# Kernel optimization log

Measured on AMD Instinct MI355X. Metric: run time of the kernel, lower is better.

The kernel has to match this reference:

```python
import jax, jax.numpy as jnp
import numpy as np

N = 50000
E = 800000
F_IN = 128
HID = 64
HEADS = 4
NEG_SLOPE = 0.2  # PyG GATConv default negative_slope


def segment_softmax(e, dst, num_segments):
    # numerically stable softmax over edges grouped by destination node
    m = jax.ops.segment_max(e, dst, num_segments=num_segments)
    ex = jnp.exp(e - m[dst])
    s = jax.ops.segment_sum(ex, dst, num_segments=num_segments)
    return ex / (s[dst] + 1e-16)


def gat_conv(x, src, dst, W, a_src, a_dst, bias, heads, out_ch, concat):
    n = x.shape[0]
    h = (x @ W).reshape(n, heads, out_ch)          # [N,H,C]
    alpha_s = (h * a_src).sum(-1)                  # [N,H]
    alpha_d = (h * a_dst).sum(-1)                  # [N,H]
    e = jax.nn.leaky_relu(alpha_s[src] + alpha_d[dst], NEG_SLOPE)  # [E,H]
    alpha = segment_softmax(e, dst, n)             # [E,H]
    out = jax.ops.segment_sum(h[src] * alpha[:, :, None], dst, num_segments=n)  # [N,H,C]
    out = out.reshape(n, heads * out_ch) if concat else out.mean(axis=1)
    return out + bias


def setup_inputs() -> dict:
    key = jax.random.key(0)
    ks = jax.random.split(key, 16)

    def lin(k, i, o):
        return (jax.random.normal(k, (i, o), jnp.float32) / np.float32(np.sqrt(i)))

    def att(k, h, c):
        return jax.random.normal(k, (h, c), jnp.float32) * np.float32(0.1)

    x = jax.random.normal(ks[0], (N, F_IN), jnp.float32)
    edge_index = jax.random.randint(ks[1], (2, E), 0, N, dtype=jnp.int32)
    return {
        "x": x,
        "W_emb": lin(ks[2], F_IN, HID), "b_emb": jnp.zeros(HID, jnp.float32),
        "W0": lin(ks[3], HID, HEADS * HID), "as0": att(ks[4], HEADS, HID), "ad0": att(ks[5], HEADS, HID), "b0": jnp.zeros(HEADS * HID, jnp.float32),
        "W1": lin(ks[6], HEADS * HID, HEADS * HID), "as1": att(ks[7], HEADS, HID), "ad1": att(ks[8], HEADS, HID), "b1": jnp.zeros(HEADS * HID, jnp.float32),
        "W2": lin(ks[9], HEADS * HID, HID), "as2": att(ks[10], 1, HID), "ad2": att(ks[11], 1, HID), "b2": jnp.zeros(HID, jnp.float32),
        "Wo1": lin(ks[12], HID, HID // 2), "bo1": jnp.zeros(HID // 2, jnp.float32),
        "Wo2": lin(ks[13], HID // 2, 1), "bo2": jnp.zeros(1, jnp.float32),
        "edge_index": edge_index,
    }


def reference(x, W_emb, b_emb, W0, as0, ad0, b0, W1, as1, ad1, b1, W2, as2, ad2, b2, Wo1, bo1, Wo2, bo2, edge_index):
    n = x.shape[0]
    loop = jnp.arange(n, dtype=edge_index.dtype)  # PyG GATConv adds self-loops
    src = jnp.concatenate([edge_index[0], loop])
    dst = jnp.concatenate([edge_index[1], loop])
    h = jax.nn.relu(x @ W_emb + b_emb)
    h = jax.nn.relu(gat_conv(h, src, dst, W0, as0, ad0, b0, HEADS, HID, True))   # dropout=identity (eval)
    h = jax.nn.relu(gat_conv(h, src, dst, W1, as1, ad1, b1, HEADS, HID, True))
    h = gat_conv(h, src, dst, W2, as2, ad2, b2, 1, HID, False)
    h = jax.nn.relu(h @ Wo1 + bo1)
    return h @ Wo2 + bo2  # [N,1]
```

## Files before the change

### kernel.cpp

```cpp
#include <hip/hip_runtime.h>

typedef _Float16 h8_t __attribute__((ext_vector_type(8)));
typedef _Float16 h4_t __attribute__((ext_vector_type(4)));
typedef float floatx4 __attribute__((ext_vector_type(4)));

__device__ __forceinline__ float leaky(float v) { return v >= 0.f ? v : 0.2f * v; }

__global__ void hist_kernel(const int* __restrict__ dst, int E, int* __restrict__ cnt) {
    int e = blockIdx.x * blockDim.x + threadIdx.x;
    if (e < E) atomicAdd(&cnt[dst[e]], 1);
}

__global__ __launch_bounds__(256) void blocksum_kernel(const int* __restrict__ cnt, int N,
                                                       int* __restrict__ bsum) {
    __shared__ int red[256];
    int tid = threadIdx.x;
    int idx = blockIdx.x * 256 + tid;
    red[tid] = idx < N ? cnt[idx] + 1 : 0;
    __syncthreads();
#pragma unroll
    for (int off = 128; off >= 1; off >>= 1) {
        if (tid < off) red[tid] += red[tid + off];
        __syncthreads();
    }
    if (tid == 0) bsum[blockIdx.x] = red[0];
}

__global__ __launch_bounds__(256) void scanbsum_kernel(int* __restrict__ bsum, int nb,
                                                       int* __restrict__ total) {
    __shared__ int part[256];
    int tid = threadIdx.x;
    int per = (nb + 255) / 256;
    int s0 = tid * per, s1 = min(s0 + per, nb);
    int s = 0;
    for (int i = s0; i < s1; i++) s += bsum[i];
    part[tid] = s;
    __syncthreads();
    for (int off = 1; off < 256; off <<= 1) {
        int v = (tid >= off) ? part[tid - off] : 0;
        __syncthreads();
        part[tid] += v;
        __syncthreads();
    }
    int base = (tid == 0) ? 0 : part[tid - 1];
    for (int i = s0; i < s1; i++) {
        int v = bsum[i];
        bsum[i] = base;
        base += v;
    }
    if (tid == 255) *total = part[255];
}

__global__ __launch_bounds__(256) void rowptr_kernel(const int* __restrict__ cnt,
                                                     const int* __restrict__ bsum, int N,
                                                     int* __restrict__ row_ptr,
                                                     int* __restrict__ cursor) {
    __shared__ int lds[256];
    int tid = threadIdx.x;
    int idx = blockIdx.x * 256 + tid;
    int v = idx < N ? cnt[idx] + 1 : 0;
    lds[tid] = v;
    __syncthreads();
    for (int off = 1; off < 256; off <<= 1) {
        int t = (tid >= off) ? lds[tid - off] : 0;
        __syncthreads();
        lds[tid] += t;
        __syncthreads();
    }
    if (idx < N) {
        int p = bsum[blockIdx.x] + lds[tid] - v;
        row_ptr[idx] = p;
        cursor[idx] = p;
    }
}

__global__ void scatter_kernel(const int* __restrict__ src, const int* __restrict__ dst,
                               int E, int N, int* __restrict__ cursor, int* __restrict__ csr_src) {
    int e = blockIdx.x * blockDim.x + threadIdx.x;
    if (e >= E + N) return;
    int s, d;
    if (e < E) { s = src[e]; d = dst[e]; }
    else       { s = e - E;  d = s; }
    int pos = atomicAdd(&cursor[d], 1);
    csr_src[pos] = s;
}

__global__ void prep_weights_all(const float* __restrict__ W_emb, const float* __restrict__ W0,
                                 const float* __restrict__ W1, const float* __restrict__ W2,
                                 _Float16* __restrict__ WeH, _Float16* __restrict__ WeL,
                                 _Float16* __restrict__ W0H, _Float16* __restrict__ W0L,
                                 _Float16* __restrict__ W1H, _Float16* __restrict__ W1L,
                                 _Float16* __restrict__ W2H, _Float16* __restrict__ W2L) {
    int which = blockIdx.y;
    const float* W;
    _Float16 *Wh, *Wl;
    int K, N;
    if (which == 0)      { W = W_emb; Wh = WeH; Wl = WeL; K = 128; N = 64; }
    else if (which == 1) { W = W0;    Wh = W0H; Wl = W0L; K = 64;  N = 256; }
    else if (which == 2) { W = W1;    Wh = W1H; Wl = W1L; K = 256; N = 256; }
    else                 { W = W2;    Wh = W2H; Wl = W2L; K = 256; N = 64; }
    int idx = blockIdx.x * blockDim.x + threadIdx.x;
    if (idx >= K * N) return;
    int k = idx / N, n = idx % N;
    float v = W[idx];
    _Float16 hi = (_Float16)v;
    _Float16 lo = (_Float16)(v - (float)hi);
    size_t o = ((size_t)(k >> 3) * N + n) * 8 + (k & 7);
    Wh[o] = hi; Wl[o] = lo;
}

__global__ __launch_bounds__(256) void gemm_emb_kernel(
        const float* __restrict__ X,
        const _Float16* __restrict__ Bh, const _Float16* __restrict__ Bl,
        const float* __restrict__ bias,
        _Float16* __restrict__ Ph, _Float16* __restrict__ Pl,
        int Mpad, int M) {
    const int Nn = 64, K = 128;
    __shared__ _Float16 Bs[2][16][64][8];
    __shared__ _Float16 stH[4][16][72];
    __shared__ _Float16 stL[4][16][72];
    int tid = threadIdx.x;
    int wv = tid >> 6, lane = tid & 63;
    int m16 = lane & 15, quad = lane >> 4;
    int row0 = blockIdx.x * 128 + wv * 32;

#pragma unroll
    for (int cc = 0; cc < 8; cc++) {
        int c = tid + cc * 256;
        int plane = c >> 10, rem = c & 1023, q = rem >> 6, col = rem & 63;
        const _Float16* srcp = (plane ? Bl : Bh) + ((size_t)q * Nn + col) * 8;
        *reinterpret_cast<h8_t*>(&Bs[plane][q][col][0]) = *reinterpret_cast<const h8_t*>(srcp);
    }
    __syncthreads();

    floatx4 acc[2][4];
#pragma unroll
    for (int t = 0; t < 2; t++)
#pragma unroll
        for (int c = 0; c < 4; c++)
#pragma unroll
            for (int i = 0; i < 4; i++) acc[t][c][i] = 0.f;

    int r0 = row0 + m16, r1 = row0 + 16 + m16;
#pragma unroll
    for (int kt4 = 0; kt4 < 4; kt4++) {
        int kcol = kt4 * 32 + quad * 8;
        float vs0[8] = {0,0,0,0,0,0,0,0}, vs1[8] = {0,0,0,0,0,0,0,0};
        if (r0 < M) {
            const float4* p = (const float4*)(X + (size_t)r0 * K + kcol);
            float4 a = p[0], b = p[1];
            vs0[0]=a.x; vs0[1]=a.y; vs0[2]=a.z; vs0[3]=a.w;
            vs0[4]=b.x; vs0[5]=b.y; vs0[6]=b.z; vs0[7]=b.w;
        }
        if (r1 < M) {
            const float4* p = (const float4*)(X + (size_t)r1 * K + kcol);
            float4 a = p[0], b = p[1];
            vs1[0]=a.x; vs1[1]=a.y; vs1[2]=a.z; vs1[3]=a.w;
            vs1[4]=b.x; vs1[5]=b.y; vs1[6]=b.z; vs1[7]=b.w;
        }
        h8_t ah0, al0, ah1, al1;
#pragma unroll
        for (int j = 0; j < 8; j++) {
            _Float16 hi0 = (_Float16)vs0[j];
            ah0[j] = hi0; al0[j] = (_Float16)(vs0[j] - (float)hi0);
            _Float16 hi1 = (_Float16)vs1[j];
            ah1[j] = hi1; al1[j] = (_Float16)(vs1[j] - (float)hi1);
        }
        int kq = kt4 * 4 + quad;
#pragma unroll
        for (int c = 0; c < 4; c++) {
            h8_t bh = *reinterpret_cast<const h8_t*>(&Bs[0][kq][c * 16 + m16][0]);
            h8_t bl = *reinterpret_cast<const h8_t*>(&Bs[1][kq][c * 16 + m16][0]);
            acc[0][c] = __builtin_amdgcn_mfma_f32_16x16x32_f16(ah0, bh, acc[0][c], 0, 0, 0);
            acc[1][c] = __builtin_amdgcn_mfma_f32_16x16x32_f16(ah1, bh, acc[1][c], 0, 0, 0);
            acc[0][c] = __builtin_amdgcn_mfma_f32_16x16x32_f16(ah0, bl, acc[0][c], 0, 0, 0);
            acc[1][c] = __builtin_amdgcn_mfma_f32_16x16x32_f16(ah1, bl, acc[1][c], 0, 0, 0);
            acc[0][c] = __builtin_amdgcn_mfma_f32_16x16x32_f16(al0, bh, acc[0][c], 0, 0, 0);
            acc[1][c] = __builtin_amdgcn_mfma_f32_16x16x32_f16(al1, bh, acc[1][c], 0, 0, 0);
        }
    }

#pragma unroll
    for (int t = 0; t < 2; t++) {
#pragma unroll
        for (int c = 0; c < 4; c++) {
            float bv = bias[c * 16 + m16];
#pragma unroll
            for (int i = 0; i < 4; i++) {
                float v = fmaxf(acc[t][c][i] + bv, 0.f);
                _Float16 hi = (_Float16)v;
                stH[wv][quad * 4 + i][c * 16 + m16] = hi;
                stL[wv][quad * 4 + i][c * 16 + m16] = (_Float16)(v - (float)hi);
            }
        }
        int rowChunk = row0 + t * 16;
#pragma unroll
        for (int it = 0; it < 2; it++) {
            int lid = it * 64 + lane;
            int kg = lid >> 4, rloc = lid & 15;
            h8_t vh = *reinterpret_cast<const h8_t*>(&stH[wv][rloc][kg * 8]);
            h8_t vl = *reinterpret_cast<const h8_t*>(&stL[wv][rloc][kg * 8]);
            size_t o = ((size_t)kg * Mpad + rowChunk + rloc) * 8;
            *reinterpret_cast<h8_t*>(Ph + o) = vh;
            *reinterpret_cast<h8_t*>(Pl + o) = vl;
        }
    }
}

__global__ __launch_bounds__(256) void gemm_gat0_kernel(
        const _Float16* __restrict__ Ah, const _Float16* __restrict__ Al,
        const _Float16* __restrict__ Bh, const _Float16* __restrict__ Bl,
        const float* __restrict__ a_src, const float* __restrict__ a_dst,
        _Float16* __restrict__ hOut, float* __restrict__ aS, float* __restrict__ aD,
        int Mpad, int M) {
    const int Nn = 256;
    __shared__ _Float16 Bs[2][8][128][8];
    __shared__ _Float16 st[4][16][136];
    int tid = threadIdx.x;
    int wv = tid >> 6, lane = tid & 63;
    int m16 = lane & 15, quad = lane >> 4;
    int row0 = blockIdx.y * 128 + wv * 32;
    int colBase = blockIdx.x * 128;
    size_t kqbase = (size_t)colBase * 8;

#pragma unroll
    for (int cc = 0; cc < 8; cc++) {
        int c = tid + cc * 256;
        int plane = c >> 10, rem = c & 1023, q = rem >> 7, col = rem & 127;
        const _Float16* srcp = (plane ? Bl : Bh) + kqbase + ((size_t)q * Nn + col) * 8;
        *reinterpret_cast<h8_t*>(&Bs[plane][q][col][0]) = *reinterpret_cast<const h8_t*>(srcp);
    }
    __syncthreads();

    floatx4 acc[2][8];
#pragma unroll
    for (int t = 0; t < 2; t++)
#pragma unroll
        for (int c = 0; c < 8; c++)
#pragma unroll
            for (int i = 0; i < 4; i++) acc[t][c][i] = 0.f;

#pragma unroll
    for (int kt = 0; kt < 2; kt++) {
        int kq = kt * 4 + quad;
        size_t aoff = ((size_t)kq * Mpad + row0 + m16) * 8;
        h8_t ah0 = *reinterpret_cast<const h8_t*>(Ah + aoff);
        h8_t ah1 = *reinterpret_cast<const h8_t*>(Ah + aoff + 128);
        h8_t al0 = *reinterpret_cast<const h8_t*>(Al + aoff);
        h8_t al1 = *reinterpret_cast<const h8_t*>(Al + aoff + 128);
#pragma unroll
        for (int c = 0; c < 8; c++) {
            h8_t bh = *reinterpret_cast<const h8_t*>(&Bs[0][kq][c * 16 + m16][0]);
            h8_t bl = *reinterpret_cast<const h8_t*>(&Bs[1][kq][c * 16 + m16][0]);
            acc[0][c] = __builtin_amdgcn_mfma_f32_16x16x32_f16(ah0, bh, acc[0][c], 0, 0, 0);
            acc[1][c] = __builtin_amdgcn_mfma_f32_16x16x32_f16(ah1, bh, acc[1][c], 0, 0, 0);
            acc[0][c] = __builtin_amdgcn_mfma_f32_16x16x32_f16(ah0, bl, acc[0][c], 0, 0, 0);
            acc[1][c] = __builtin_amdgcn_mfma_f32_16x16x32_f16(ah1, bl, acc[1][c], 0, 0, 0);
            acc[0][c] = __builtin_amdgcn_mfma_f32_16x16x32_f16(al0, bh, acc[0][c], 0, 0, 0);
            acc[1][c] = __builtin_amdgcn_mfma_f32_16x16x32_f16(al1, bh, acc[1][c], 0, 0, 0);
        }
    }

    float asv[8], adv[8];
#pragma unroll
    for (int c = 0; c < 8; c++) {
        asv[c] = a_src[colBase + c * 16 + m16];
        adv[c] = a_dst[colBase + c * 16 + m16];
    }
    int hb = colBase >> 6;
#pragma unroll
    for (int t = 0; t < 2; t++) {
#pragma unroll
        for (int i = 0; i < 4; i++) {
            int r = row0 + t * 16 + quad * 4 + i;
            float s0 = 0.f, d0 = 0.f, s1 = 0.f, d1 = 0.f;
#pragma unroll
            for (int c = 0; c < 8; c++) {
                float v = acc[t][c][i];
                if (c < 4) { s0 += v * asv[c]; d0 += v * adv[c]; }
                else       { s1 += v * asv[c]; d1 += v * adv[c]; }
            }
#pragma unroll
            for (int off = 1; off < 16; off <<= 1) {
                s0 += __shfl_xor(s0, off);
                d0 += __shfl_xor(d0, off);
                s1 += __shfl_xor(s1, off);
                d1 += __shfl_xor(d1, off);
            }
            if (m16 == 0 && r < M) {
                aS[r * 4 + hb] = s0;     aD[r * 4 + hb] = d0;
                aS[r * 4 + hb + 1] = s1; aD[r * 4 + hb + 1] = d1;
            }
        }
    }

#pragma unroll
    for (int t = 0; t < 2; t++) {
#pragma unroll
        for (int c = 0; c < 8; c++)
#pragma unroll
            for (int i = 0; i < 4; i++)
                st[wv][quad * 4 + i][c * 16 + m16] = (_Float16)acc[t][c][i];
        int rowChunk = row0 + t * 16;
#pragma unroll
        for (int it = 0; it < 4; it++) {
            int lid = it * 64 + lane;
            int rloc = lid >> 4, u = lid & 15;
            h8_t v = *reinterpret_cast<const h8_t*>(&st[wv][rloc][u * 8]);
            *reinterpret_cast<h8_t*>(hOut + (size_t)(rowChunk + rloc) * 256 + colBase + u * 8) = v;
        }
    }
}

__global__ __launch_bounds__(256) void gemm_gat1_kernel(
        const _Float16* __restrict__ Ah, const _Float16* __restrict__ Al,
        const _Float16* __restrict__ Bh, const _Float16* __restrict__ Bl,
        const float* __restrict__ a_src, const float* __restrict__ a_dst,
        _Float16* __restrict__ hOut, float* __restrict__ aS, float* __restrict__ aD,
        int Mpad, int M, int K) {
    const int Nn = 256;
    __shared__ _Float16 Bs[2][4][128][8];
    __shared__ _Float16 st[4][16][136];
    int tid = threadIdx.x;
    int wv = tid >> 6, lane = tid & 63;
    int m16 = lane & 15, quad = lane >> 4;
    int row0 = blockIdx.y * 128 + wv * 32;
    int colBase = blockIdx.x * 128;

    floatx4 acc[2][8];
#pragma unroll
    for (int t = 0; t < 2; t++)
#pragma unroll
        for (int c = 0; c < 8; c++)
#pragma unroll
            for (int i = 0; i < 4; i++) acc[t][c][i] = 0.f;

    int sPlane[4], sQ[4], sCol[4];
    const _Float16* sBase[4];
#pragma unroll
    for (int cc = 0; cc < 4; cc++) {
        int c = tid + cc * 256;
        sPlane[cc] = c >> 9;
        int rem = c & 511;
        sQ[cc] = rem >> 7;
        sCol[cc] = rem & 127;
        sBase[cc] = (sPlane[cc] ? Bl : Bh) + ((size_t)sQ[cc] * Nn + sCol[cc]) * 8;
    }

    size_t aoff = ((size_t)quad * Mpad + row0 + m16) * 8;
    size_t kqbase = (size_t)colBase * 8;
    const size_t aStep = (size_t)Mpad * 32;
    const size_t bStep = (size_t)Nn * 32;

    h8_t aR[4], bR[4];
    aR[0] = *reinterpret_cast<const h8_t*>(Ah + aoff);
    aR[1] = *reinterpret_cast<const h8_t*>(Ah + aoff + 128);
    aR[2] = *reinterpret_cast<const h8_t*>(Al + aoff);
    aR[3] = *reinterpret_cast<const h8_t*>(Al + aoff + 128);
#pragma unroll
    for (int cc = 0; cc < 4; cc++)
        bR[cc] = *reinterpret_cast<const h8_t*>(sBase[cc] + kqbase);

    for (int kt = 0; kt < K; kt += 32) {
#pragma unroll
        for (int cc = 0; cc < 4; cc++)
            *reinterpret_cast<h8_t*>(&Bs[sPlane[cc]][sQ[cc]][sCol[cc]][0]) = bR[cc];
        __syncthreads();
        h8_t aN[4], bN[4];
        bool more = (kt + 32) < K;
        if (more) {
            aoff += aStep; kqbase += bStep;
            aN[0] = *reinterpret_cast<const h8_t*>(Ah + aoff);
            aN[1] = *reinterpret_cast<const h8_t*>(Ah + aoff + 128);
            aN[2] = *reinterpret_cast<const h8_t*>(Al + aoff);
            aN[3] = *reinterpret_cast<const h8_t*>(Al + aoff + 128);
#pragma unroll
            for (int cc = 0; cc < 4; cc++)
                bN[cc] = *reinterpret_cast<const h8_t*>(sBase[cc] + kqbase);
        }
#pragma unroll
        for (int c = 0; c < 8; c++) {
            h8_t bh = *reinterpret_cast<const h8_t*>(&Bs[0][quad][c * 16 + m16][0]);
            h8_t bl = *reinterpret_cast<const h8_t*>(&Bs[1][quad][c * 16 + m16][0]);
            acc[0][c] = __builtin_amdgcn_mfma_f32_16x16x32_f16(aR[0], bh, acc[0][c], 0, 0, 0);
            acc[1][c] = __builtin_amdgcn_mfma_f32_16x16x32_f16(aR[1], bh, acc[1][c], 0, 0, 0);
            acc[0][c] = __builtin_amdgcn_mfma_f32_16x16x32_f16(aR[0], bl, acc[0][c], 0, 0, 0);
            acc[1][c] = __builtin_amdgcn_mfma_f32_16x16x32_f16(aR[1], bl, acc[1][c], 0, 0, 0);
            acc[0][c] = __builtin_amdgcn_mfma_f32_16x16x32_f16(aR[2], bh, acc[0][c], 0, 0, 0);
            acc[1][c] = __builtin_amdgcn_mfma_f32_16x16x32_f16(aR[3], bh, acc[1][c], 0, 0, 0);
        }
        __syncthreads();
        if (more) {
#pragma unroll
            for (int j = 0; j < 4; j++) { aR[j] = aN[j]; bR[j] = bN[j]; }
        }
    }

    float asv[8], adv[8];
#pragma unroll
    for (int c = 0; c < 8; c++) {
        asv[c] = a_src[colBase + c * 16 + m16];
        adv[c] = a_dst[colBase + c * 16 + m16];
    }
    int hb = colBase >> 6;
#pragma unroll
    for (int t = 0; t < 2; t++) {
#pragma unroll
        for (int i = 0; i < 4; i++) {
            int r = row0 + t * 16 + quad * 4 + i;
            float s0 = 0.f, d0 = 0.f, s1 = 0.f, d1 = 0.f;
#pragma unroll
            for (int c = 0; c < 8; c++) {
                float v = acc[t][c][i];
                if (c < 4) { s0 += v * asv[c]; d0 += v * adv[c]; }
                else       { s1 += v * asv[c]; d1 += v * adv[c]; }
            }
#pragma unroll
            for (int off = 1; off < 16; off <<= 1) {
                s0 += __shfl_xor(s0, off);
                d0 += __shfl_xor(d0, off);
                s1 += __shfl_xor(s1, off);
                d1 += __shfl_xor(d1, off);
            }
            if (m16 == 0 && r < M) {
                aS[r * 4 + hb] = s0;     aD[r * 4 + hb] = d0;
                aS[r * 4 + hb + 1] = s1; aD[r * 4 + hb + 1] = d1;
            }
        }
    }

#pragma unroll
    for (int t = 0; t < 2; t++) {
#pragma unroll
        for (int c = 0; c < 8; c++)
#pragma unroll
            for (int i = 0; i < 4; i++)
                st[wv][quad * 4 + i][c * 16 + m16] = (_Float16)acc[t][c][i];
        int rowChunk = row0 + t * 16;
#pragma unroll
        for (int it = 0; it < 4; it++) {
            int lid = it * 64 + lane;
            int rloc = lid >> 4, u = lid & 15;
            h8_t v = *reinterpret_cast<const h8_t*>(&st[wv][rloc][u * 8]);
            *reinterpret_cast<h8_t*>(hOut + (size_t)(rowChunk + rloc) * 256 + colBase + u * 8) = v;
        }
    }
}

__global__ __launch_bounds__(256) void gemm_l2_kernel(
        const _Float16* __restrict__ Ah, const _Float16* __restrict__ Al,
        const _Float16* __restrict__ Bh, const _Float16* __restrict__ Bl,
        const float* __restrict__ a_src, const float* __restrict__ a_dst,
        _Float16* __restrict__ hOut, float* __restrict__ aS, float* __restrict__ aD,
        int Mpad, int M, int K) {
    const int Nn = 64;
    __shared__ _Float16 Bs[2][4][64][8];
    __shared__ _Float16 st[4][16][72];
    int tid = threadIdx.x;
    int wv = tid >> 6, lane = tid & 63;
    int m16 = lane & 15, quad = lane >> 4;
    int row0 = blockIdx.x * 128 + wv * 32;

    floatx4 acc[2][4];
#pragma unroll
    for (int t = 0; t < 2; t++)
#pragma unroll
        for (int c = 0; c < 4; c++)
#pragma unroll
            for (int i = 0; i < 4; i++) acc[t][c][i] = 0.f;

    int sPlane[2], sQ[2], sCol[2];
    const _Float16* sBase[2];
#pragma unroll
    for (int cc = 0; cc < 2; cc++) {
        int c = tid + cc * 256;
        sPlane[cc] = c >> 8;
        int rem = c & 255;
        sQ[cc] = rem >> 6;
        sCol[cc] = rem & 63;
        sBase[cc] = (sPlane[cc] ? Bl : Bh) + ((size_t)sQ[cc] * Nn + sCol[cc]) * 8;
    }

    size_t aoff = ((size_t)quad * Mpad + row0 + m16) * 8;
    size_t kqbase = 0;
    const size_t aStep = (size_t)Mpad * 32;
    const size_t bStep = (size_t)Nn * 32;

    h8_t aR[4], bR[2];
    aR[0] = *reinterpret_cast<const h8_t*>(Ah + aoff);
    aR[1] = *reinterpret_cast<const h8_t*>(Ah + aoff + 128);
    aR[2] = *reinterpret_cast<const h8_t*>(Al + aoff);
    aR[3] = *reinterpret_cast<const h8_t*>(Al + aoff + 128);
#pragma unroll
    for (int cc = 0; cc < 2; cc++)
        bR[cc] = *reinterpret_cast<const h8_t*>(sBase[cc] + kqbase);

    for (int kt = 0; kt < K; kt += 32) {
#pragma unroll
        for (int cc = 0; cc < 2; cc++)
            *reinterpret_cast<h8_t*>(&Bs[sPlane[cc]][sQ[cc]][sCol[cc]][0]) = bR[cc];
        __syncthreads();
        h8_t aN[4], bN[2];
        bool more = (kt + 32) < K;
        if (more) {
            aoff += aStep; kqbase += bStep;
            aN[0] = *reinterpret_cast<const h8_t*>(Ah + aoff);
            aN[1] = *reinterpret_cast<const h8_t*>(Ah + aoff + 128);
            aN[2] = *reinterpret_cast<const h8_t*>(Al + aoff);
            aN[3] = *reinterpret_cast<const h8_t*>(Al + aoff + 128);
#pragma unroll
            for (int cc = 0; cc < 2; cc++)
                bN[cc] = *reinterpret_cast<const h8_t*>(sBase[cc] + kqbase);
        }
#pragma unroll
        for (int c = 0; c < 4; c++) {
            h8_t bh = *reinterpret_cast<const h8_t*>(&Bs[0][quad][c * 16 + m16][0]);
            h8_t bl = *reinterpret_cast<const h8_t*>(&Bs[1][quad][c * 16 + m16][0]);
            acc[0][c] = __builtin_amdgcn_mfma_f32_16x16x32_f16(aR[0], bh, acc[0][c], 0, 0, 0);
            acc[1][c] = __builtin_amdgcn_mfma_f32_16x16x32_f16(aR[1], bh, acc[1][c], 0, 0, 0);
            acc[0][c] = __builtin_amdgcn_mfma_f32_16x16x32_f16(aR[0], bl, acc[0][c], 0, 0, 0);
            acc[1][c] = __builtin_amdgcn_mfma_f32_16x16x32_f16(aR[1], bl, acc[1][c], 0, 0, 0);
            acc[0][c] = __builtin_amdgcn_mfma_f32_16x16x32_f16(aR[2], bh, acc[0][c], 0, 0, 0);
            acc[1][c] = __builtin_amdgcn_mfma_f32_16x16x32_f16(aR[3], bh, acc[1][c], 0, 0, 0);
        }
        __syncthreads();
        if (more) {
            aR[0] = aN[0]; aR[1] = aN[1]; aR[2] = aN[2]; aR[3] = aN[3];
            bR[0] = bN[0]; bR[1] = bN[1];
        }
    }

    float asv[4], adv[4];
#pragma unroll
    for (int c = 0; c < 4; c++) {
        asv[c] = a_src[c * 16 + m16];
        adv[c] = a_dst[c * 16 + m16];
    }
#pragma unroll
    for (int t = 0; t < 2; t++) {
#pragma unroll
        for (int i = 0; i < 4; i++) {
            int r = row0 + t * 16 + quad * 4 + i;
            float s0 = 0.f, d0 = 0.f;
#pragma unroll
            for (int c = 0; c < 4; c++) {
                float v = acc[t][c][i];
                s0 += v * asv[c]; d0 += v * adv[c];
            }
#pragma unroll
            for (int off = 1; off < 16; off <<= 1) {
                s0 += __shfl_xor(s0, off);
                d0 += __shfl_xor(d0, off);
            }
            if (m16 == 0 && r < M) { aS[r] = s0; aD[r] = d0; }
        }
    }

#pragma unroll
    for (int t = 0; t < 2; t++) {
#pragma unroll
        for (int c = 0; c < 4; c++)
#pragma unroll
            for (int i = 0; i < 4; i++)
                st[wv][quad * 4 + i][c * 16 + m16] = (_Float16)acc[t][c][i];
        int rowChunk = row0 + t * 16;
#pragma unroll
        for (int it = 0; it < 2; it++) {
            int lid = it * 64 + lane;
            int rloc = lid >> 3, u = lid & 7;
            h8_t v = *reinterpret_cast<const h8_t*>(&st[wv][rloc][u * 8]);
            *reinterpret_cast<h8_t*>(hOut + (size_t)(rowChunk + rloc) * 64 + u * 8) = v;
        }
    }
}

template <int TAG>
__global__ __launch_bounds__(256) void aggregate4_kernel(const _Float16* __restrict__ hsrc,
                                                         const float* __restrict__ alpha_s,
                                                         const float* __restrict__ alpha_d,
                                                         const int* __restrict__ row_ptr,
                                                         const int* __restrict__ csr_src,
                                                         const float* __restrict__ bias,
                                                         _Float16* __restrict__ outH,
                                                         _Float16* __restrict__ outL,
                                                         int N, int Mpad) {
    __shared__ float wlds[4][64][4];
    __shared__ int   slds[4][64];
    int wv = threadIdx.x >> 6, lane = threadIdx.x & 63;
    int node = blockIdx.x * 4 + wv;
    if (node >= N) return;
    int rs = row_ptr[node], re = row_ptr[node + 1];
    int slot = lane >> 5, lp = lane & 31;
    int ghead = lp >> 3;
    int gbyte = lp * 16;
    float4 ad4 = *(const float4*)(alpha_d + (size_t)node * 4);

    float den0 = 0.f, den1 = 0.f, den2 = 0.f, den3 = 0.f;
    float acc8[8] = {0.f, 0.f, 0.f, 0.f, 0.f, 0.f, 0.f, 0.f};
    float* wp = &wlds[wv][0][0];
    int*   sp = &slds[wv][0];
    const char* hbase = (const char*)hsrc;
    for (int base = rs; base < re; base += 64) {
        int i = base + lane;
        float w0 = 0.f, w1 = 0.f, w2 = 0.f, w3 = 0.f;
        int off = 0;
        if (i < re) {
            int s = __builtin_nontemporal_load(csr_src + i);
            float4 as = *(const float4*)(alpha_s + (size_t)s * 4);
            w0 = __expf(fminf(leaky(as.x + ad4.x), 60.f));
            w1 = __expf(fminf(leaky(as.y + ad4.y), 60.f));
            w2 = __expf(fminf(leaky(as.z + ad4.z), 60.f));
            w3 = __expf(fminf(leaky(as.w + ad4.w), 60.f));
            off = s * 512;
        }
        den0 += w0; den1 += w1; den2 += w2; den3 += w3;
        sp[lane] = off;
        *(float4*)(wp + lane * 4) = make_float4(w0, w1, w2, w3);
        int cnt = min(64, re - base);
#pragma unroll 2
        for (int j = slot; j < cnt; j += 2) {
            int o2 = sp[j];
            float w = wp[j * 4 + ghead];
            h8_t hv = *reinterpret_cast<const h8_t*>(hbase + o2 + gbyte);
#pragma unroll
            for (int k = 0; k < 8; k++) acc8[k] += w * (float)hv[k];
        }
    }
#pragma unroll
    for (int k = 0; k < 8; k++) acc8[k] += __shfl_xor(acc8[k], 32);
#pragma unroll
    for (int off = 32; off >= 1; off >>= 1) {
        den0 += __shfl_xor(den0, off);
        den1 += __shfl_xor(den1, off);
        den2 += __shfl_xor(den2, off);
        den3 += __shfl_xor(den3, off);
    }
    if (slot == 0) {
        float den = (ghead & 2) ? ((ghead & 1) ? den3 : den2) : ((ghead & 1) ? den1 : den0);
        float inv = 1.f / (den + 1e-16f);
        int cbase = lp * 8;
        float4 b0 = *(const float4*)(bias + cbase);
        float4 b1 = *(const float4*)(bias + cbase + 4);
        float bv[8] = {b0.x, b0.y, b0.z, b0.w, b1.x, b1.y, b1.z, b1.w};
        h8_t hv, lv;
#pragma unroll
        for (int k = 0; k < 8; k++) {
            float v = fmaxf(acc8[k] * inv + bv[k], 0.f);
            _Float16 hi = (_Float16)v;
            hv[k] = hi;
            lv[k] = (_Float16)(v - (float)hi);
        }
        size_t o = ((size_t)lp * Mpad + node) * 8;
        *reinterpret_cast<h8_t*>(outH + o) = hv;
        *reinterpret_cast<h8_t*>(outL + o) = lv;
    }
}

__global__ __launch_bounds__(256) void agg1_mlp_kernel(const _Float16* __restrict__ hsrc,
                                                       const float* __restrict__ alpha_s,
                                                       const float* __restrict__ alpha_d,
                                                       const int* __restrict__ row_ptr,
                                                       const int* __restrict__ csr_src,
                                                       const float* __restrict__ bias,
                                                       const float* __restrict__ Wo1,
                                                       const float* __restrict__ bo1,
                                                       const float* __restrict__ Wo2,
                                                       const float* __restrict__ bo2,
                                                       float* __restrict__ out, int N) {
    __shared__ float wlds[4][64];
    __shared__ int   slds[4][64];
    __shared__ float hrow[4][64];
    __shared__ float w1s[64 * 32];
    __shared__ float w2s[32];
    __shared__ float b1s[32];
    int tid = threadIdx.x;
#pragma unroll
    for (int i = 0; i < 8; i++) w1s[tid + i * 256] = Wo1[tid + i * 256];
    if (tid < 32) { w2s[tid] = Wo2[tid]; b1s[tid] = bo1[tid]; }
    __syncthreads();

    int wv = tid >> 6, lane = tid & 63;
    int node = blockIdx.x * 4 + wv;
    if (node >= N) return;
    int rs = row_ptr[node], re = row_ptr[node + 1];
    float ad = alpha_d[node];
    int slot = lane >> 3, lp = lane & 7;
    int gbyte = lp * 16;

    float den = 0.f;
    float acc8[8] = {0.f, 0.f, 0.f, 0.f, 0.f, 0.f, 0.f, 0.f};
    const char* hbase = (const char*)hsrc;
    float* wp = &wlds[wv][0];
    int*   sp = &slds[wv][0];
    for (int base = rs; base < re; base += 64) {
        int i = base + lane;
        float w = 0.f;
        int off = 0;
        if (i < re) {
            int s = __builtin_nontemporal_load(csr_src + i);
            w = __expf(fminf(leaky(alpha_s[s] + ad), 60.f));
            off = s * 128;
        }
        den += w;
        sp[lane] = off;
        wp[lane] = w;
        int cnt = min(64, re - base);
#pragma unroll 2
        for (int j = slot; j < cnt; j += 8) {
            float wj = wp[j];
            h8_t hv = *reinterpret_cast<const h8_t*>(hbase + sp[j] + gbyte);
#pragma unroll
            for (int k = 0; k < 8; k++) acc8[k] += wj * (float)hv[k];
        }
    }
#pragma unroll
    for (int k = 0; k < 8; k++) {
        acc8[k] += __shfl_xor(acc8[k], 8);
        acc8[k] += __shfl_xor(acc8[k], 16);
        acc8[k] += __shfl_xor(acc8[k], 32);
    }
#pragma unroll
    for (int off = 32; off >= 1; off >>= 1) den += __shfl_xor(den, off);
    if (slot == 0) {
        float inv = 1.f / (den + 1e-16f);
        int cbase = lp * 8;
#pragma unroll
        for (int k = 0; k < 8; k++)
            hrow[wv][cbase + k] = acc8[k] * inv + bias[cbase + k];
    }
    int j = lane & 31;
    float a = b1s[j];
#pragma unroll 4
    for (int k = 0; k < 64; k++) a += hrow[wv][k] * w1s[k * 32 + j];
    a = fmaxf(a, 0.f);
    float p = a * w2s[j];
#pragma unroll
    for (int off = 16; off >= 1; off >>= 1) p += __shfl_xor(p, off);
    if (lane == 0) out[node] = p + bo2[0];
}

extern "C" void kernel_launch(void* const* d_in, const int* in_sizes, int n_in,
                              void* d_out, int out_size, void* d_ws, size_t ws_size,
                              hipStream_t stream) {
    const float* x     = (const float*)d_in[0];
    const float* W_emb = (const float*)d_in[1];
    const float* b_emb = (const float*)d_in[2];
    const float* W0    = (const float*)d_in[3];
    const float* as0   = (const float*)d_in[4];
    const float* ad0   = (const float*)d_in[5];
    const float* b0    = (const float*)d_in[6];
    const float* W1    = (const float*)d_in[7];
    const float* as1   = (const float*)d_in[8];
    const float* ad1   = (const float*)d_in[9];
    const float* b1    = (const float*)d_in[10];
    const float* W2    = (const float*)d_in[11];
    const float* as2   = (const float*)d_in[12];
    const float* ad2   = (const float*)d_in[13];
    const float* b2    = (const float*)d_in[14];
    const float* Wo1   = (const float*)d_in[15];
    const float* bo1   = (const float*)d_in[16];
    const float* Wo2   = (const float*)d_in[17];
    const float* bo2   = (const float*)d_in[18];
    const int* eidx    = (const int*)d_in[19];

    const int N = in_sizes[0] / 128;
    const int E = in_sizes[19] / 2;
    const int* esrc = eidx;
    const int* edst = eidx + E;
    const int gmB  = (N + 127) / 128;
    const int Mpad = gmB * 128;
    const int nb   = (N + 255) / 256;

    char* w = (char*)d_ws;
    auto alloc = [&](size_t bytes) {
        char* p = w;
        w += (bytes + 255) & ~(size_t)255;
        return (void*)p;
    };
    _Float16* hOut = (_Float16*)alloc((size_t)Mpad * 256 * 2);
    _Float16* PHh  = (_Float16*)alloc((size_t)Mpad * 256 * 2);
    _Float16* PHl  = (_Float16*)alloc((size_t)Mpad * 256 * 2);
    float* aS      = (float*)alloc((size_t)N * 4 * 4);
    float* aD      = (float*)alloc((size_t)N * 4 * 4);
    int*   row_ptr = (int*)alloc((size_t)(N + 1) * 4);
    int*   cursor  = (int*)alloc((size_t)N * 4);
    int*   cnt     = (int*)alloc((size_t)N * 4);
    int*   bsum    = (int*)alloc((size_t)nb * 4);
    int*   csr     = (int*)alloc((size_t)(E + N) * 4);
    _Float16* WeH  = (_Float16*)alloc(128 * 64 * 2);
    _Float16* WeL  = (_Float16*)alloc(128 * 64 * 2);
    _Float16* W0H  = (_Float16*)alloc(64 * 256 * 2);
    _Float16* W0L  = (_Float16*)alloc(64 * 256 * 2);
    _Float16* W1H  = (_Float16*)alloc(256 * 256 * 2);
    _Float16* W1L  = (_Float16*)alloc(256 * 256 * 2);
    _Float16* W2H  = (_Float16*)alloc(256 * 64 * 2);
    _Float16* W2L  = (_Float16*)alloc(256 * 64 * 2);

    hipMemsetAsync(cnt, 0, (size_t)N * 4, stream);
    hist_kernel<<<(E + 255) / 256, 256, 0, stream>>>(edst, E, cnt);
    blocksum_kernel<<<nb, 256, 0, stream>>>(cnt, N, bsum);
    scanbsum_kernel<<<1, 256, 0, stream>>>(bsum, nb, row_ptr + N);
    rowptr_kernel<<<nb, 256, 0, stream>>>(cnt, bsum, N, row_ptr, cursor);
    scatter_kernel<<<(E + N + 255) / 256, 256, 0, stream>>>(esrc, edst, E, N, cursor, csr);

    prep_weights_all<<<dim3(256, 4), 256, 0, stream>>>(W_emb, W0, W1, W2,
                                                       WeH, WeL, W0H, W0L, W1H, W1L, W2H, W2L);

    int gn4 = (N + 3) / 4;

    gemm_emb_kernel<<<dim3(gmB, 1), 256, 0, stream>>>(x, WeH, WeL, b_emb, PHh, PHl, Mpad, N);

    gemm_gat0_kernel<<<dim3(2, gmB), 256, 0, stream>>>(PHh, PHl, W0H, W0L, as0, ad0, hOut, aS, aD, Mpad, N);
    aggregate4_kernel<0><<<gn4, 256, 0, stream>>>(hOut, aS, aD, row_ptr, csr, b0, PHh, PHl, N, Mpad);

    gemm_gat1_kernel<<<dim3(2, gmB), 256, 0, stream>>>(PHh, PHl, W1H, W1L, as1, ad1, hOut, aS, aD, Mpad, N, 256);
    aggregate4_kernel<1><<<gn4, 256, 0, stream>>>(hOut, aS, aD, row_ptr, csr, b1, PHh, PHl, N, Mpad);

    gemm_l2_kernel<<<dim3(gmB, 1), 256, 0, stream>>>(PHh, PHl, W2H, W2L, as2, ad2, hOut, aS, aD, Mpad, N, 256);
    agg1_mlp_kernel<<<gn4, 256, 0, stream>>>(hOut, aS, aD, row_ptr, csr, b2,
                                             Wo1, bo1, Wo2, bo2, (float*)d_out, N);
}
```

Baseline: 484.5 us.

## Split 4-head aggregation across two blocks per node by head pair

The aggregation kernel for the 4-head GAT layers now launches two blocks per group of nodes, each handling two of the four heads (128 channels) instead of all 256 channels. Each wave processes four edges at a time with 16 lanes per edge rather than two edges with 32 lanes, which doubles the number of in-flight gathers per wave and raises parallelism for low-degree nodes. In exchange, the CSR indices and alpha_s values are read twice, the exp work is split but repeated per block, and there are extra shuffles for the reduction.

```diff
diff --git a/kernel.cpp b/kernel.cpp
--- a/kernel.cpp
+++ b/kernel.cpp
@@ -584,63 +584,63 @@
                                                          _Float16* __restrict__ outH,
                                                          _Float16* __restrict__ outL,
                                                          int N, int Mpad) {
-    __shared__ float wlds[4][64][4];
+    __shared__ float wlds[4][64][2];
     __shared__ int   slds[4][64];
-    int wv = threadIdx.x >> 6, lane = threadIdx.x & 63;
-    int node = blockIdx.x * 4 + wv;
+    int tid = threadIdx.x;
+    int wv = tid >> 6, lane = tid & 63;
+    int grp = blockIdx.x & 1;
+    int node = (blockIdx.x >> 1) * 4 + wv;
     if (node >= N) return;
     int rs = row_ptr[node], re = row_ptr[node + 1];
-    int slot = lane >> 5, lp = lane & 31;
+    int slot = lane >> 4, lp = lane & 15;
     int ghead = lp >> 3;
-    int gbyte = lp * 16;
-    float4 ad4 = *(const float4*)(alpha_d + (size_t)node * 4);
-
-    float den0 = 0.f, den1 = 0.f, den2 = 0.f, den3 = 0.f;
+    float2 ad2 = *(const float2*)(alpha_d + (size_t)node * 4 + grp * 2);
+
+    float den0 = 0.f, den1 = 0.f;
     float acc8[8] = {0.f, 0.f, 0.f, 0.f, 0.f, 0.f, 0.f, 0.f};
     float* wp = &wlds[wv][0][0];
     int*   sp = &slds[wv][0];
-    const char* hbase = (const char*)hsrc;
+    const char* hbase = (const char*)hsrc + grp * 256;
     for (int base = rs; base < re; base += 64) {
         int i = base + lane;
-        float w0 = 0.f, w1 = 0.f, w2 = 0.f, w3 = 0.f;
+        float w0 = 0.f, w1 = 0.f;
         int off = 0;
         if (i < re) {
             int s = __builtin_nontemporal_load(csr_src + i);
-            float4 as = *(const float4*)(alpha_s + (size_t)s * 4);
-            w0 = __expf(fminf(leaky(as.x + ad4.x), 60.f));
-            w1 = __expf(fminf(leaky(as.y + ad4.y), 60.f));
-            w2 = __expf(fminf(leaky(as.z + ad4.z), 60.f));
-            w3 = __expf(fminf(leaky(as.w + ad4.w), 60.f));
+            float2 as = *(const float2*)(alpha_s + (size_t)s * 4 + grp * 2);
+            w0 = __expf(fminf(leaky(as.x + ad2.x), 60.f));
+            w1 = __expf(fminf(leaky(as.y + ad2.y), 60.f));
             off = s * 512;
         }
-        den0 += w0; den1 += w1; den2 += w2; den3 += w3;
+        den0 += w0; den1 += w1;
         sp[lane] = off;
-        *(float4*)(wp + lane * 4) = make_float4(w0, w1, w2, w3);
+        *(float2*)(wp + lane * 2) = make_float2(w0, w1);
         int cnt = min(64, re - base);
 #pragma unroll 2
-        for (int j = slot; j < cnt; j += 2) {
+        for (int j = slot; j < cnt; j += 4) {
             int o2 = sp[j];
-            float w = wp[j * 4 + ghead];
-            h8_t hv = *reinterpret_cast<const h8_t*>(hbase + o2 + gbyte);
+            float w = wp[j * 2 + ghead];
+            h8_t hv = *reinterpret_cast<const h8_t*>(hbase + o2 + lp * 16);
 #pragma unroll
             for (int k = 0; k < 8; k++) acc8[k] += w * (float)hv[k];
         }
     }
 #pragma unroll
-    for (int k = 0; k < 8; k++) acc8[k] += __shfl_xor(acc8[k], 32);
+    for (int k = 0; k < 8; k++) {
+        acc8[k] += __shfl_xor(acc8[k], 16);
+        acc8[k] += __shfl_xor(acc8[k], 32);
+    }
 #pragma unroll
     for (int off = 32; off >= 1; off >>= 1) {
         den0 += __shfl_xor(den0, off);
         den1 += __shfl_xor(den1, off);
-        den2 += __shfl_xor(den2, off);
-        den3 += __shfl_xor(den3, off);
     }
     if (slot == 0) {
-        float den = (ghead & 2) ? ((ghead & 1) ? den3 : den2) : ((ghead & 1) ? den1 : den0);
+        float den = ghead ? den1 : den0;
         float inv = 1.f / (den + 1e-16f);
-        int cbase = lp * 8;
-        float4 b0 = *(const float4*)(bias + cbase);
-        float4 b1 = *(const float4*)(bias + cbase + 4);
+        int ch0 = grp * 128 + lp * 8;
+        float4 b0 = *(const float4*)(bias + ch0);
+        float4 b1 = *(const float4*)(bias + ch0 + 4);
         float bv[8] = {b0.x, b0.y, b0.z, b0.w, b1.x, b1.y, b1.z, b1.w};
         h8_t hv, lv;
 #pragma unroll
@@ -650,7 +650,8 @@
             hv[k] = hi;
             lv[k] = (_Float16)(v - (float)hi);
         }
-        size_t o = ((size_t)lp * Mpad + node) * 8;
+        int kq = grp * 16 + lp;
+        size_t o = ((size_t)kq * Mpad + node) * 8;
         *reinterpret_cast<h8_t*>(outH + o) = hv;
         *reinterpret_cast<h8_t*>(outL + o) = lv;
     }
@@ -807,14 +808,15 @@
                                                        WeH, WeL, W0H, W0L, W1H, W1L, W2H, W2L);
 
     int gn4 = (N + 3) / 4;
+    int gnAgg = gn4 * 2;
 
     gemm_emb_kernel<<<dim3(gmB, 1), 256, 0, stream>>>(x, WeH, WeL, b_emb, PHh, PHl, Mpad, N);
 
     gemm_gat0_kernel<<<dim3(2, gmB), 256, 0, stream>>>(PHh, PHl, W0H, W0L, as0, ad0, hOut, aS, aD, Mpad, N);
-    aggregate4_kernel<0><<<gn4, 256, 0, stream>>>(hOut, aS, aD, row_ptr, csr, b0, PHh, PHl, N, Mpad);
+    aggregate4_kernel<0><<<gnAgg, 256, 0, stream>>>(hOut, aS, aD, row_ptr, csr, b0, PHh, PHl, N, Mpad);
 
     gemm_gat1_kernel<<<dim3(2, gmB), 256, 0, stream>>>(PHh, PHl, W1H, W1L, as1, ad1, hOut, aS, aD, Mpad, N, 256);
-    aggregate4_kernel<1><<<gn4, 256, 0, stream>>>(hOut, aS, aD, row_ptr, csr, b1, PHh, PHl, N, Mpad);
+    aggregate4_kernel<1><<<gnAgg, 256, 0, stream>>>(hOut, aS, aD, row_ptr, csr, b1, PHh, PHl, N, Mpad);
 
     gemm_l2_kernel<<<dim3(gmB, 1), 256, 0, stream>>>(PHh, PHl, W2H, W2L, as2, ad2, hOut, aS, aD, Mpad, N, 256);
     agg1_mlp_kernel<<<gn4, 256, 0, stream>>>(hOut, aS, aD, row_ptr, csr, b2,
```

New measurement: 482.1 us. About the same (-0.5%).
